# Kernel tuning notes

Hardware: AMD Instinct MI355X
Metric: run time of the kernel (lower is better)

Reference implementation:

```python
import jax, jax.numpy as jnp
import numpy as np

B, N, D, H, K = 8, 128, 256, 128, 8

def setup_inputs() -> dict:
    key = jax.random.key(0)
    ks = jax.random.split(key, 6)
    E = jax.random.normal(ks[0], (B, N, D), dtype=jnp.float32)
    # kaiming_uniform-like init for linear weights
    lim1 = np.sqrt(6.0 / (2 * D))
    W1 = jax.random.uniform(ks[1], (H, 2 * D), minval=-lim1, maxval=lim1, dtype=jnp.float32)
    b1 = jnp.zeros((H,), dtype=jnp.float32)
    lim2 = np.sqrt(6.0 / H)
    W2 = jax.random.uniform(ks[2], (D, H), minval=-lim2, maxval=lim2, dtype=jnp.float32)
    b2 = jnp.zeros((D,), dtype=jnp.float32)
    q = jax.random.normal(ks[3], (K, D), dtype=jnp.float32) * (1.0 / D ** 0.5)
    return {"E": E, "W1": W1, "b1": b1, "W2": W2, "b2": b2, "q": q}

def reference(E, W1, b1, W2, b2, q):
    # phi(cat(Ei,Ej)) == relu(E_i @ W1a^T + E_j @ W1b^T + b1) @ W2^T + b2
    # Split first linear's weight to avoid materializing the [B,N,N,2D] concat.
    W1a, W1b = W1[:, :D], W1[:, D:]          # each [H, D]
    Ai = jnp.einsum('bnd,hd->bnh', E, W1a)   # [B,N,H] (row half)
    Aj = jnp.einsum('bnd,hd->bnh', E, W1b)   # [B,N,H] (col half)
    hidden = jax.nn.relu(Ai[:, :, None, :] + Aj[:, None, :, :] + b1)  # [B,N,N,H]
    # dropout is identity at inference
    # Fuse second linear with query dot: (hidden @ W2^T + b2) . q_h
    #   = hidden @ (W2^T q_h) + b2.q_h
    Wq = jnp.einsum('dh,kd->hk', W2, q)      # [H, K]
    bq = jnp.einsum('d,kd->k', b2, q)        # [K]
    logits = jnp.einsum('bijh,hk->bijh'[:0] or 'bijh,hk->bijk', hidden, Wq) + bq  # [B,N,N,K]
    M = jax.nn.sigmoid(logits).transpose(0, 3, 1, 2)  # [B,K,N,N]
    eye = jnp.eye(N, dtype=M.dtype)[None, None]
    return M * (1.0 - eye)
```

## Files before the change

### kernel.cpp

```cpp
#include <hip/hip_runtime.h>

#define PB 8
#define PN 128
#define PD 256
#define PH 128
#define PK 8
#define D2 (2*PD)
#define NT 4

__global__ __launch_bounds__(256) void k1_proj(
        const float* __restrict__ E,  const float* __restrict__ W1,
        const float* __restrict__ b1, const float* __restrict__ W2,
        const float* __restrict__ b2, const float* __restrict__ q,
        float* __restrict__ Ai, float* __restrict__ Ajt,
        float* __restrict__ Wq, float* __restrict__ bq)
{
    const int blk = blockIdx.x, t = threadIdx.x;

    if (blk < 512) {
        __shared__ float es[NT][PD];
        __shared__ float wtile[32][PH + 1];
        const int b    = blk >> 6;
        const int rest = blk & 63;
        const int n0   = (rest >> 1) * NT;
        const int part = rest & 1;
        const int h    = t & (PH - 1);
        const int s    = t >> 7;

        const float* erow = E + (b * PN + n0) * PD;
        float* esf = &es[0][0];
        #pragma unroll
        for (int r = 0; r < 4; ++r) esf[r * 256 + t] = erow[r * 256 + t];

        const int na = n0 + 2 * s;
        float acca = 0.f, accb = 0.f;
        const float* w1row = W1 + h * D2 + part * PD;

        for (int dc = 0; dc < 8; ++dc) {
            __syncthreads();
            const int cb = dc * 32 + s * 16;
            #pragma unroll
            for (int qq = 0; qq < 4; ++qq) {
                float4 v = *reinterpret_cast<const float4*>(w1row + cb + qq * 4);
                const int ld = s * 16 + qq * 4;
                wtile[ld + 0][h] = v.x;
                wtile[ld + 1][h] = v.y;
                wtile[ld + 2][h] = v.z;
                wtile[ld + 3][h] = v.w;
            }
            __syncthreads();
            const int dbase = dc * 32;
            #pragma unroll
            for (int g = 0; g < 8; ++g) {
                const float w0 = wtile[g * 4 + 0][h];
                const float w1v = wtile[g * 4 + 1][h];
                const float w2v = wtile[g * 4 + 2][h];
                const float w3v = wtile[g * 4 + 3][h];
                float4 ea = *reinterpret_cast<const float4*>(&es[2 * s + 0][dbase + g * 4]);
                float4 eb = *reinterpret_cast<const float4*>(&es[2 * s + 1][dbase + g * 4]);
                acca = fmaf(w0, ea.x, acca); acca = fmaf(w1v, ea.y, acca);
                acca = fmaf(w2v, ea.z, acca); acca = fmaf(w3v, ea.w, acca);
                accb = fmaf(w0, eb.x, accb); accb = fmaf(w1v, eb.y, accb);
                accb = fmaf(w2v, eb.z, accb); accb = fmaf(w3v, eb.w, accb);
            }
        }

        if (part == 0) {
            const float bb = b1[h];
            Ai[(b * PN + na) * PH + h]     = acca + bb;
            Ai[(b * PN + na + 1) * PH + h] = accb + bb;
        } else {
            *reinterpret_cast<float2*>(&Ajt[(b * PH + h) * PN + na]) =
                make_float2(acca, accb);
        }
    } else {
        __shared__ float qs[PD];
        __shared__ float red[256];
        const int k = blk - 512;
        qs[t] = q[k * PD + t];
        __syncthreads();
        if (t < PH) {
            float acc = 0.f;
            #pragma unroll 4
            for (int d = 0; d < PD; ++d)
                acc = fmaf(W2[d * PH + t], qs[d], acc);
            Wq[t * PK + k] = acc;
        }
        red[t] = b2[t] * qs[t];
        __syncthreads();
        for (int st = 128; st > 0; st >>= 1) {
            if (t < st) red[t] += red[t + st];
            __syncthreads();
        }
        if (t == 0) bq[k] = red[0];
    }
}

__global__ __launch_bounds__(256) void k2_score(
        const float* __restrict__ Ai, const float* __restrict__ Ajt,
        const float* __restrict__ Wq, const float* __restrict__ bq,
        float* __restrict__ out)
{
    __shared__ float wq[PH * PK];
    __shared__ float ais[2 * PH];
    __shared__ float bqs[PK];

    const int blk = blockIdx.x, t = threadIdx.x;
    const int b  = blk >> 6;
    const int i0 = (blk & 63) << 1;

    *reinterpret_cast<float4*>(&wq[t * 4]) =
        *reinterpret_cast<const float4*>(&Wq[t * 4]);
    ais[t] = Ai[(b * PN + i0) * PH + t];
    if (t < PK) bqs[t] = bq[t];
    __syncthreads();

    const int half = t >> 7;
    const int i = i0 + half;
    const int j = t & (PN - 1);
    const float* ail = ais + half * PH;
    const float* aj = Ajt + b * PH * PN + j;

    float acc[PK];
    #pragma unroll
    for (int k = 0; k < PK; ++k) acc[k] = bqs[k];

    #pragma unroll 4
    for (int h = 0; h < PH; ++h) {
        const float v = fmaxf(ail[h] + aj[h * PN], 0.f);
        float4 w0 = *reinterpret_cast<const float4*>(&wq[h * PK]);
        float4 w1 = *reinterpret_cast<const float4*>(&wq[h * PK + 4]);
        acc[0] = fmaf(v, w0.x, acc[0]); acc[1] = fmaf(v, w0.y, acc[1]);
        acc[2] = fmaf(v, w0.z, acc[2]); acc[3] = fmaf(v, w0.w, acc[3]);
        acc[4] = fmaf(v, w1.x, acc[4]); acc[5] = fmaf(v, w1.y, acc[5]);
        acc[6] = fmaf(v, w1.z, acc[6]); acc[7] = fmaf(v, w1.w, acc[7]);
    }

    #pragma unroll
    for (int k = 0; k < PK; ++k) {
        float s = 1.f / (1.f + __expf(-acc[k]));
        if (j == i) s = 0.f;
        out[((b * PK + k) * PN + i) * PN + j] = s;
    }
}

extern "C" void kernel_launch(void* const* d_in, const int* in_sizes, int n_in,
                              void* d_out, int out_size, void* d_ws, size_t ws_size,
                              hipStream_t stream) {
    const float* E  = (const float*)d_in[0];
    const float* W1 = (const float*)d_in[1];
    const float* b1 = (const float*)d_in[2];
    const float* W2 = (const float*)d_in[3];
    const float* b2 = (const float*)d_in[4];
    const float* q  = (const float*)d_in[5];

    float* Ai  = (float*)d_ws;
    float* Ajt = Ai + PB * PN * PH;
    float* Wq  = Ajt + PB * PN * PH;
    float* bq  = Wq + PH * PK;

    k1_proj<<<520, 256, 0, stream>>>(E, W1, b1, W2, b2, q, Ai, Ajt, Wq, bq);
    k2_score<<<PB * PN / 2, 256, 0, stream>>>(Ai, Ajt, Wq, bq, (float*)d_out);
}
```

Before: 99.48 us.

## Split score kernel over K halves and widen projection weight tiles

The score kernel now launches twice as many blocks, and each one computes only 4 of the 8 K outputs. This gives more parallelism across the 256 CUs, at the cost of recomputing the relu(hidden) values and re-reading Ajt twice. The projection kernel doubles its W1 shared tile to 64 rows, halving the number of sync iterations, and sets a launch-bounds occupancy hint.

```diff
diff --git a/kernel.cpp b/kernel.cpp
--- a/kernel.cpp
+++ b/kernel.cpp
@@ -8,7 +8,7 @@
 #define D2 (2*PD)
 #define NT 4
 
-__global__ __launch_bounds__(256) void k1_proj(
+__global__ __launch_bounds__(256, 2) void k1_proj(
         const float* __restrict__ E,  const float* __restrict__ W1,
         const float* __restrict__ b1, const float* __restrict__ W2,
         const float* __restrict__ b2, const float* __restrict__ q,
@@ -19,7 +19,7 @@
 
     if (blk < 512) {
         __shared__ float es[NT][PD];
-        __shared__ float wtile[32][PH + 1];
+        __shared__ float wtile[64][PH + 1];
         const int b    = blk >> 6;
         const int rest = blk & 63;
         const int n0   = (rest >> 1) * NT;
@@ -36,23 +36,23 @@
         float acca = 0.f, accb = 0.f;
         const float* w1row = W1 + h * D2 + part * PD;
 
-        for (int dc = 0; dc < 8; ++dc) {
+        for (int dc = 0; dc < 4; ++dc) {
             __syncthreads();
-            const int cb = dc * 32 + s * 16;
+            const int cb = dc * 64 + s * 32;
             #pragma unroll
-            for (int qq = 0; qq < 4; ++qq) {
+            for (int qq = 0; qq < 8; ++qq) {
                 float4 v = *reinterpret_cast<const float4*>(w1row + cb + qq * 4);
-                const int ld = s * 16 + qq * 4;
+                const int ld = s * 32 + qq * 4;
                 wtile[ld + 0][h] = v.x;
                 wtile[ld + 1][h] = v.y;
                 wtile[ld + 2][h] = v.z;
                 wtile[ld + 3][h] = v.w;
             }
             __syncthreads();
-            const int dbase = dc * 32;
+            const int dbase = dc * 64;
             #pragma unroll
-            for (int g = 0; g < 8; ++g) {
-                const float w0 = wtile[g * 4 + 0][h];
+            for (int g = 0; g < 16; ++g) {
+                const float w0  = wtile[g * 4 + 0][h];
                 const float w1v = wtile[g * 4 + 1][h];
                 const float w2v = wtile[g * 4 + 2][h];
                 const float w3v = wtile[g * 4 + 3][h];
@@ -101,18 +101,21 @@
         const float* __restrict__ Wq, const float* __restrict__ bq,
         float* __restrict__ out)
 {
-    __shared__ float wq[PH * PK];
+    __shared__ float wqh[PH * 4];
     __shared__ float ais[2 * PH];
-    __shared__ float bqs[PK];
+    __shared__ float bqs[4];
 
     const int blk = blockIdx.x, t = threadIdx.x;
-    const int b  = blk >> 6;
-    const int i0 = (blk & 63) << 1;
+    const int b  = blk >> 7;
+    const int r  = blk & 127;
+    const int i0 = (r >> 1) << 1;
+    const int kh = r & 1;
 
-    *reinterpret_cast<float4*>(&wq[t * 4]) =
-        *reinterpret_cast<const float4*>(&Wq[t * 4]);
+    if (t < PH)
+        *reinterpret_cast<float4*>(&wqh[t * 4]) =
+            *reinterpret_cast<const float4*>(&Wq[t * PK + 4 * kh]);
     ais[t] = Ai[(b * PN + i0) * PH + t];
-    if (t < PK) bqs[t] = bq[t];
+    if (t < 4) bqs[t] = bq[4 * kh + t];
     __syncthreads();
 
     const int half = t >> 7;
@@ -121,26 +124,23 @@
     const float* ail = ais + half * PH;
     const float* aj = Ajt + b * PH * PN + j;
 
-    float acc[PK];
+    float acc[4];
     #pragma unroll
-    for (int k = 0; k < PK; ++k) acc[k] = bqs[k];
+    for (int k = 0; k < 4; ++k) acc[k] = bqs[k];
 
-    #pragma unroll 4
+    #pragma unroll 8
     for (int h = 0; h < PH; ++h) {
         const float v = fmaxf(ail[h] + aj[h * PN], 0.f);
-        float4 w0 = *reinterpret_cast<const float4*>(&wq[h * PK]);
-        float4 w1 = *reinterpret_cast<const float4*>(&wq[h * PK + 4]);
+        float4 w0 = *reinterpret_cast<const float4*>(&wqh[h * 4]);
         acc[0] = fmaf(v, w0.x, acc[0]); acc[1] = fmaf(v, w0.y, acc[1]);
         acc[2] = fmaf(v, w0.z, acc[2]); acc[3] = fmaf(v, w0.w, acc[3]);
-        acc[4] = fmaf(v, w1.x, acc[4]); acc[5] = fmaf(v, w1.y, acc[5]);
-        acc[6] = fmaf(v, w1.z, acc[6]); acc[7] = fmaf(v, w1.w, acc[7]);
     }
 
     #pragma unroll
-    for (int k = 0; k < PK; ++k) {
+    for (int k = 0; k < 4; ++k) {
         float s = 1.f / (1.f + __expf(-acc[k]));
         if (j == i) s = 0.f;
-        out[((b * PK + k) * PN + i) * PN + j] = s;
+        out[((b * PK + 4 * kh + k) * PN + i) * PN + j] = s;
     }
 }
 
@@ -160,5 +160,5 @@
     float* bq  = Wq + PH * PK;
 
     k1_proj<<<520, 256, 0, stream>>>(E, W1, b1, W2, b2, q, Ai, Ajt, Wq, bq);
-    k2_score<<<PB * PN / 2, 256, 0, stream>>>(Ai, Ajt, Wq, bq, (float*)d_out);
+    k2_score<<<PB * PN, 256, 0, stream>>>(Ai, Ajt, Wq, bq, (float*)d_out);
 }
```

Measured after the change: 97.05 us. 2.4% less time.
